# Kernel optimization log

Measured on AMD Instinct MI355X. Metric: run time of the kernel, lower is better.

## Reference

```python
import jax, jax.numpy as jnp
import numpy as np

K = 3          # k_size
STRIDE = 2
LAMDA = 10.0
PAD = K // 2
EPS = 1e-6


def _unfold(x, k, s, pad):
    # x: [B,C,H,W] -> [B, C*k*k, L]; matches torch.nn.functional.unfold ordering
    x = jnp.pad(x, ((0, 0), (0, 0), (pad, pad), (pad, pad)))
    B, C, Hp, Wp = x.shape
    Ho = (Hp - k) // s + 1
    Wo = (Wp - k) // s + 1
    # stack k*k shifted strided views -> [B, C, k*k, Ho, Wo], kk index = i*k + j
    cols = jnp.stack([x[:, :, i:i + s * (Ho - 1) + 1:s, j:j + s * (Wo - 1) + 1:s]
                      for i in range(k) for j in range(k)], axis=2)
    return cols.reshape(B, C * k * k, Ho * Wo)


def setup_inputs() -> dict:
    key = jax.random.key(0)
    k0, k1, k2, k3 = jax.random.split(key, 4)
    B, C, H, W = 4, 64, 64, 64
    bg_in = jax.random.normal(k0, (B, C, H, W), dtype=jnp.float32)
    fg_in = jax.random.normal(k1, (B, C, H, W), dtype=jnp.float32)
    mask = (jax.random.uniform(k2, (B, 1, H, W)) > 0.5).astype(jnp.float32)
    fuse_w = jax.random.normal(k3, (C, 2 * C, 1, 1), dtype=jnp.float32) * 0.02
    fuse_b = jnp.zeros((C,), dtype=jnp.float32)
    return {"bg_in": bg_in, "fg_in": fg_in, "mask": mask,
            "fuse_w": fuse_w, "fuse_b": fuse_b}


def reference(bg_in, fg_in, mask, fuse_w, fuse_b):
    B, C, H, W = bg_in.shape
    # mask is already [B,1,H,W] -> nearest resize is identity; expand over channels
    mask_r = jnp.broadcast_to(mask, (B, C, H, W))
    bg = bg_in * mask_r

    ub = _unfold(bg, K, STRIDE, 0)              # [B, d, L], d = C*K*K (bg patches = keys)
    L = ub.shape[-1]
    uf = _unfold(fg_in, K, 1, PAD)              # [B, d, H*W] (fg patches = queries)
    ww = uf.transpose(0, 2, 1).reshape(B, H, W, C * K * K)  # [B,H,W,d]

    k1d = jnp.sum(ub ** 2, axis=1)                       # [B,L]   ||key||^2
    wwd = jnp.sum(ww ** 2, axis=-1, keepdims=True)       # [B,H,W,1] ||query||^2
    CS = jnp.einsum('bhwd,bdl->bhwl', ww, ub)            # cross-correlation
    DS1 = k1d[:, None, None, :] + wwd - 2.0 * CS         # squared L2 distances [B,H,W,L]

    mean = DS1.mean(axis=-1, keepdims=True)
    std = DS1.std(axis=-1, keepdims=True)                # ddof=0 == unbiased=False
    DS2 = -jnp.tanh((DS1 - mean) / (std + EPS))
    CA = jax.nn.softmax(LAMDA * DS2, axis=-1)            # attention over L patches

    # conv_transpose2d(CA, k2, stride=1, padding=PAD): scatter-add of weighted patches
    k2 = ub.transpose(0, 2, 1).reshape(B, L, C, K, K)    # per-batch deconv weights
    T = jnp.einsum('bhwl,blcij->bchwij', CA, k2)         # [B,C,H,W,K,K]
    outp = jnp.zeros((B, C, H + 2 * PAD, W + 2 * PAD), dtype=bg_in.dtype)
    for i in range(K):
        for j in range(K):
            outp = outp.at[:, :, i:i + H, j:j + W].add(T[:, :, :, :, i, j])
    ACL = outp[:, :, PAD:PAD + H, PAD:PAD + W] / (K * K)

    ACL = bg + ACL * (1.0 - mask_r)
    con1 = jnp.concatenate([bg_in, ACL], axis=1)         # [B,2C,H,W]
    out = jnp.einsum('bdhw,cd->bchw', con1, fuse_w[:, :, 0, 0]) + fuse_b[None, :, None, None]
    return jax.nn.elu(out)
```

## Files before the change

### kernel.cpp

```cpp
#include <hip/hip_runtime.h>

#define B_   4
#define C_   64
#define HW_  4096
#define D_   576
#define L_   961
#define LP_  1024
#define LAMDA_ 10.0f
#define EPS_   1e-6f

typedef short short8 __attribute__((ext_vector_type(8)));
typedef float f32x16 __attribute__((ext_vector_type(16)));
typedef unsigned short u16;

__device__ __forceinline__ u16 f2bf(float x) {
    unsigned u = __float_as_uint(x);
    u += 0x7FFFu + ((u >> 16) & 1u);
    return (u16)(u >> 16);
}
__device__ __forceinline__ float bf2f(u16 h) {
    return __uint_as_float(((unsigned)h) << 16);
}
__device__ __forceinline__ void mfma_bf16(f32x16& d, short8 a, short8 b) {
    asm volatile("v_mfma_f32_32x32x16_bf16 %0, %1, %2, %0"
                 : "+v"(d) : "v"(a), "v"(b));
}

__global__ __launch_bounds__(256) void fill_ub_kernel(const float* __restrict__ bg_in,
                                                      const float* __restrict__ mask,
                                                      u16* __restrict__ UBh,
                                                      u16* __restrict__ UBl) {
    int idx = blockIdx.x * 256 + threadIdx.x;
    int b   = idx / (D_ * LP_);
    int rem = idx - b * (D_ * LP_);
    int d   = rem >> 10;
    int l   = idx & (LP_ - 1);
    float v = 0.f;
    if (l < L_) {
        int ly = l / 31, lx = l - ly * 31;
        int c  = d / 9,  kk = d - c * 9;
        int i  = kk / 3, j  = kk - i * 3;
        int pix = ((2 * ly + i) << 6) + 2 * lx + j;
        v = bg_in[((b * C_ + c) << 12) + pix] * mask[(b << 12) + pix];
    }
    u16 h = f2bf(v);
    UBh[idx] = h;
    UBl[idx] = f2bf(v - bf2f(h));
}

__global__ __launch_bounds__(256) void fill_ubT_kernel(const float* __restrict__ bg_in,
                                                       const float* __restrict__ mask,
                                                       u16* __restrict__ UBTh,
                                                       u16* __restrict__ UBTl) {
    int idx = blockIdx.x * 256 + threadIdx.x;
    int d   = idx % D_;
    int tmp = idx / D_;
    int l   = tmp & (LP_ - 1);
    int b   = tmp >> 10;
    float v = 0.f;
    if (l < L_) {
        int ly = l / 31, lx = l - ly * 31;
        int c  = d / 9,  kk = d - c * 9;
        int i  = kk / 3, j  = kk - i * 3;
        int pix = ((2 * ly + i) << 6) + 2 * lx + j;
        v = bg_in[((b * C_ + c) << 12) + pix] * mask[(b << 12) + pix];
    }
    u16 h = f2bf(v);
    UBTh[idx] = h;
    UBTl[idx] = f2bf(v - bf2f(h));
}

__global__ __launch_bounds__(256) void k1d_kernel(const u16* __restrict__ UBh,
                                                  const u16* __restrict__ UBl,
                                                  float* __restrict__ K1D) {
    int t = blockIdx.x * 256 + threadIdx.x;
    int b = t >> 10;
    int l = t & 1023;
    size_t base = (size_t)b * (D_ * LP_) + (size_t)(blockIdx.y * 144) * LP_ + l;
    float s = 0.f;
    #pragma unroll 8
    for (int d = 0; d < 144; ++d) {
        float v = bf2f(UBh[base + (size_t)d * LP_]) + bf2f(UBl[base + (size_t)d * LP_]);
        s += v * v;
    }
    atomicAdd(&K1D[t], s);
}

__global__ __launch_bounds__(256) void fill_ww_kernel(const float* __restrict__ fg,
                                                      u16* __restrict__ WWh,
                                                      u16* __restrict__ WWl) {
    int idx = blockIdx.x * 256 + threadIdx.x;
    int d   = idx % D_;
    int tmp = idx / D_;
    int p   = tmp & 4095;
    int b   = tmp >> 12;
    int c   = d / 9,  kk = d - c * 9;
    int i   = kk / 3, j  = kk - i * 3;
    int y   = (p >> 6) + i - 1, x = (p & 63) + j - 1;
    float v = 0.f;
    if ((unsigned)y < 64u && (unsigned)x < 64u)
        v = fg[((b * C_ + c) << 12) + (y << 6) + x];
    u16 h = f2bf(v);
    WWh[idx] = h;
    WWl[idx] = f2bf(v - bf2f(h));
}

__global__ __launch_bounds__(256) void pixsq_kernel(const float* __restrict__ fg,
                                                    float* __restrict__ P) {
    int t = blockIdx.x * 256 + threadIdx.x;
    int b = t >> 12, p = t & 4095;
    const float* base = fg + ((size_t)(b * C_) << 12) + p;
    float s = 0.f;
    #pragma unroll 8
    for (int c = 0; c < C_; ++c) { float v = base[c << 12]; s += v * v; }
    P[t] = s;
}

__global__ __launch_bounds__(256) void gemm1_kernel(
    const u16* __restrict__ WWh, const u16* __restrict__ WWl,
    const u16* __restrict__ UBTh, const u16* __restrict__ UBTl,
    float* __restrict__ CS)
{
    int b = blockIdx.z;
    const u16* Ahg = WWh  + (size_t)b * HW_ * D_;
    const u16* Alg = WWl  + (size_t)b * HW_ * D_;
    const u16* Bhg = UBTh + (size_t)b * LP_ * D_;
    const u16* Blg = UBTl + (size_t)b * LP_ * D_;
    float* C = CS + (size_t)b * HW_ * LP_;
    int n0 = blockIdx.x << 7, m0 = blockIdx.y << 7;

    __shared__ __align__(16) u16 Ah[4096], Al[4096], Bh[4096], Bl[4096];

    int t = threadIdx.x;
    int lane = t & 63;
    int w = t >> 6, wm = w >> 1, wn = w & 1;
    int lr = lane & 31, lk = lane >> 5;

    f32x16 acc[2][2];
    #pragma unroll
    for (int i = 0; i < 2; ++i)
        #pragma unroll
        for (int j = 0; j < 2; ++j)
            #pragma unroll
            for (int r = 0; r < 16; ++r) acc[i][j][r] = 0.f;

    for (int k0 = 0; k0 < D_; k0 += 32) {
        __syncthreads();
        #pragma unroll
        for (int i = 0; i < 2; ++i) {
            int lin = i * 256 + t;
            int q = lin >> 7, r = lin & 127;
            size_t ga = (size_t)(m0 + r) * D_ + k0 + q * 8;
            size_t gb = (size_t)(n0 + r) * D_ + k0 + q * 8;
            *(uint4*)&Ah[lin * 8] = *(const uint4*)(Ahg + ga);
            *(uint4*)&Al[lin * 8] = *(const uint4*)(Alg + ga);
            *(uint4*)&Bh[lin * 8] = *(const uint4*)(Bhg + gb);
            *(uint4*)&Bl[lin * 8] = *(const uint4*)(Blg + gb);
        }
        __syncthreads();
        #pragma unroll
        for (int kh = 0; kh < 2; ++kh) {
            int qq = kh * 2 + lk;
            short8 ah[2], al[2], bhf[2], blf[2];
            #pragma unroll
            for (int f = 0; f < 2; ++f) {
                int ra = (qq * 128 + wm * 64 + f * 32 + lr) * 8;
                int rb = (qq * 128 + wn * 64 + f * 32 + lr) * 8;
                ah[f]  = *(const short8*)&Ah[ra];
                al[f]  = *(const short8*)&Al[ra];
                bhf[f] = *(const short8*)&Bh[rb];
                blf[f] = *(const short8*)&Bl[rb];
            }
            #pragma unroll
            for (int fm = 0; fm < 2; ++fm)
                #pragma unroll
                for (int fn = 0; fn < 2; ++fn)
                    mfma_bf16(acc[fm][fn], ah[fm], bhf[fn]);
            #pragma unroll
            for (int fm = 0; fm < 2; ++fm)
                #pragma unroll
                for (int fn = 0; fn < 2; ++fn)
                    mfma_bf16(acc[fm][fn], ah[fm], blf[fn]);
            #pragma unroll
            for (int fm = 0; fm < 2; ++fm)
                #pragma unroll
                for (int fn = 0; fn < 2; ++fn)
                    mfma_bf16(acc[fm][fn], al[fm], bhf[fn]);
        }
    }
    #pragma unroll
    for (int fm = 0; fm < 2; ++fm)
        #pragma unroll
        for (int fn = 0; fn < 2; ++fn) {
            int colb = n0 + wn * 64 + fn * 32 + lr;
            int rowb = m0 + wm * 64 + fm * 32 + 4 * lk;
            #pragma unroll
            for (int r = 0; r < 16; ++r) {
                int row = rowb + (r & 3) + 8 * (r >> 2);
                C[(size_t)row * LP_ + colb] = acc[fm][fn][r];
            }
        }
}

__device__ __forceinline__ float block_reduce_sum(float v, float* sred) {
    #pragma unroll
    for (int m = 32; m > 0; m >>= 1) v += __shfl_xor(v, m, 64);
    __syncthreads();
    if ((threadIdx.x & 63) == 0) sred[threadIdx.x >> 6] = v;
    __syncthreads();
    return sred[0] + sred[1] + sred[2] + sred[3];
}

__global__ __launch_bounds__(256) void stats_softmax_kernel(float* __restrict__ CA,
                                                            const float* __restrict__ K1D,
                                                            const float* __restrict__ P) {
    __shared__ float sred[4];
    int row = blockIdx.x;
    int b = row >> 12, q = row & 4095;
    int h = q >> 6, wx = q & 63;
    float wwd = 0.f;
    #pragma unroll
    for (int i = 0; i < 3; ++i)
        #pragma unroll
        for (int j = 0; j < 3; ++j) {
            int y = h + i - 1, x = wx + j - 1;
            if ((unsigned)y < 64u && (unsigned)x < 64u)
                wwd += P[(b << 12) + (y << 6) + x];
        }
    float* cs = CA + (size_t)row * LP_;
    u16* ch = (u16*)cs;
    const float* k1 = K1D + (b << 10);
    int t = threadIdx.x;
    float xv[4];
    float lsum = 0.f;
    #pragma unroll
    for (int i = 0; i < 4; ++i) {
        int l = t + (i << 8);
        float ds = 0.f;
        if (l < L_) ds = k1[l] + wwd - 2.f * cs[l];
        xv[i] = ds;
        lsum += ds;
    }
    float mean = block_reduce_sum(lsum, sred) * (1.f / 961.f);
    float lvar = 0.f;
    #pragma unroll
    for (int i = 0; i < 4; ++i) {
        int l = t + (i << 8);
        if (l < L_) { float dd = xv[i] - mean; lvar += dd * dd; }
    }
    float var = block_reduce_sum(lvar, sred) * (1.f / 961.f);
    float inv = 1.f / (sqrtf(var) + EPS_);
    float ev[4];
    float lsume = 0.f;
    #pragma unroll
    for (int i = 0; i < 4; ++i) {
        int l = t + (i << 8);
        float e = 0.f;
        if (l < L_) e = expf(-LAMDA_ * tanhf((xv[i] - mean) * inv));
        ev[i] = e;
        lsume += e;
    }
    float rs = 1.f / block_reduce_sum(lsume, sred);
    #pragma unroll
    for (int i = 0; i < 4; ++i) {
        int l2 = t + (i << 8);
        float v = ev[i] * rs;
        u16 hi = f2bf(v);
        ch[l2]        = hi;
        ch[1024 + l2] = f2bf(v - bf2f(hi));
    }
}

__global__ __launch_bounds__(256) void gemm2_kernel(
    const u16* __restrict__ UBh, const u16* __restrict__ UBl,
    const float* __restrict__ CAbase, float* __restrict__ ET)
{
    int b = blockIdx.z;
    const u16* Ahg = UBh + (size_t)b * D_ * LP_;
    const u16* Alg = UBl + (size_t)b * D_ * LP_;
    const u16* CAB = (const u16*)(CAbase + (size_t)b * HW_ * LP_);
    float* C = ET + (size_t)b * D_ * HW_;
    int n0 = blockIdx.x << 8, m0 = blockIdx.y << 6;

    __shared__ __align__(16) u16 Ah[2048], Al[2048], Bh[8192], Bl[8192];

    int t = threadIdx.x;
    int lane = t & 63;
    int w = t >> 6;
    int lr = lane & 31, lk = lane >> 5;

    f32x16 acc[2][2];
    #pragma unroll
    for (int i = 0; i < 2; ++i)
        #pragma unroll
        for (int j = 0; j < 2; ++j)
            #pragma unroll
            for (int r = 0; r < 16; ++r) acc[i][j][r] = 0.f;

    for (int k0 = 0; k0 < LP_; k0 += 32) {
        __syncthreads();
        {
            int q = t >> 6, r = t & 63;
            size_t ga = (size_t)(m0 + r) * LP_ + k0 + q * 8;
            *(uint4*)&Ah[t * 8] = *(const uint4*)(Ahg + ga);
            *(uint4*)&Al[t * 8] = *(const uint4*)(Alg + ga);
        }
        #pragma unroll
        for (int i = 0; i < 4; ++i) {
            int lin = i * 256 + t;
            int q = lin >> 8, r = lin & 255;
            size_t gb = (size_t)(n0 + r) * 2048 + k0 + q * 8;
            *(uint4*)&Bh[lin * 8] = *(const uint4*)(CAB + gb);
            *(uint4*)&Bl[lin * 8] = *(const uint4*)(CAB + gb + 1024);
        }
        __syncthreads();
        #pragma unroll
        for (int kh = 0; kh < 2; ++kh) {
            int qq = kh * 2 + lk;
            short8 ah[2], al[2], bhf[2], blf[2];
            #pragma unroll
            for (int f = 0; f < 2; ++f) {
                int ra = (qq * 64 + f * 32 + lr) * 8;
                int rb = (qq * 256 + w * 64 + f * 32 + lr) * 8;
                ah[f]  = *(const short8*)&Ah[ra];
                al[f]  = *(const short8*)&Al[ra];
                bhf[f] = *(const short8*)&Bh[rb];
                blf[f] = *(const short8*)&Bl[rb];
            }
            #pragma unroll
            for (int fm = 0; fm < 2; ++fm)
                #pragma unroll
                for (int fn = 0; fn < 2; ++fn)
                    mfma_bf16(acc[fm][fn], ah[fm], bhf[fn]);
            #pragma unroll
            for (int fm = 0; fm < 2; ++fm)
                #pragma unroll
                for (int fn = 0; fn < 2; ++fn)
                    mfma_bf16(acc[fm][fn], ah[fm], blf[fn]);
            #pragma unroll
            for (int fm = 0; fm < 2; ++fm)
                #pragma unroll
                for (int fn = 0; fn < 2; ++fn)
                    mfma_bf16(acc[fm][fn], al[fm], bhf[fn]);
        }
    }
    #pragma unroll
    for (int fm = 0; fm < 2; ++fm)
        #pragma unroll
        for (int fn = 0; fn < 2; ++fn) {
            int colb = n0 + w * 64 + fn * 32 + lr;
            int rowb = m0 + fm * 32 + 4 * lk;
            #pragma unroll
            for (int r = 0; r < 16; ++r) {
                int row = rowb + (r & 3) + 8 * (r >> 2);
                C[(size_t)row * HW_ + colb] = acc[fm][fn][r];
            }
        }
}

__global__ __launch_bounds__(64) void final_kernel(const float* __restrict__ ET,
                                                   const float* __restrict__ bg_in,
                                                   const float* __restrict__ mask,
                                                   const float* __restrict__ fw,
                                                   const float* __restrict__ fb,
                                                   float* __restrict__ out) {
    __shared__ float fwT[128 * 64];
    #pragma unroll 8
    for (int lin = threadIdx.x; lin < 8192; lin += 64) {
        int c = lin >> 7, c2 = lin & 127;
        fwT[(c2 << 6) + c] = fw[lin];
    }
    __syncthreads();

    int t = blockIdx.x * 64 + threadIdx.x;
    int b = t >> 12, p = t & 4095;
    int y = p >> 6, x = p & 63;
    const float* bgp = bg_in + ((size_t)(b * C_) << 12) + p;
    const float* Eb  = ET + (size_t)b * D_ * HW_;
    float m = mask[t];

    float acc[64];
    #pragma unroll
    for (int c = 0; c < 64; ++c) acc[c] = fb[c];

    for (int c2 = 0; c2 < 64; ++c2) {
        float bgv = bgp[(size_t)c2 << 12];
        float a = 0.f;
        if (m == 0.f) {
            #pragma unroll
            for (int kk = 0; kk < 9; ++kk) {
                int i = kk / 3, j = kk - (kk / 3) * 3;
                int hh = y + 1 - i, ww2 = x + 1 - j;
                if ((unsigned)hh < 64u && (unsigned)ww2 < 64u)
                    a += Eb[(size_t)(c2 * 9 + kk) * HW_ + (hh << 6) + ww2];
            }
            a *= (1.f / 9.f);
        }
        float aclv = (m != 0.f) ? bgv : a;
        const float* f1 = &fwT[c2 << 6];
        const float* f2 = &fwT[(64 + c2) << 6];
        #pragma unroll
        for (int c4 = 0; c4 < 16; ++c4) {
            float4 fa  = *(const float4*)&f1[c4 << 2];
            float4 fb4 = *(const float4*)&f2[c4 << 2];
            acc[(c4 << 2) + 0] += fa.x * bgv + fb4.x * aclv;
            acc[(c4 << 2) + 1] += fa.y * bgv + fb4.y * aclv;
            acc[(c4 << 2) + 2] += fa.z * bgv + fb4.z * aclv;
            acc[(c4 << 2) + 3] += fa.w * bgv + fb4.w * aclv;
        }
    }
    float* op = out + ((size_t)(b * C_) << 12) + p;
    #pragma unroll
    for (int c = 0; c < 64; ++c) {
        float v = acc[c];
        op[(size_t)c << 12] = v > 0.f ? v : expm1f(v);
    }
}

extern "C" void kernel_launch(void* const* d_in, const int* in_sizes, int n_in,
                              void* d_out, int out_size, void* d_ws, size_t ws_size,
                              hipStream_t stream) {
    const float* bg_in  = (const float*)d_in[0];
    const float* fg_in  = (const float*)d_in[1];
    const float* mask   = (const float*)d_in[2];
    const float* fuse_w = (const float*)d_in[3];
    const float* fuse_b = (const float*)d_in[4];
    float* out = (float*)d_out;

    char* base = (char*)d_ws;
    u16* WWh  = (u16*)base;  base += (size_t)B_ * HW_ * D_ * 2;
    u16* WWl  = (u16*)base;  base += (size_t)B_ * HW_ * D_ * 2;
    u16* UBh  = (u16*)base;  base += (size_t)B_ * D_ * LP_ * 2;
    u16* UBl  = (u16*)base;  base += (size_t)B_ * D_ * LP_ * 2;
    u16* UBTh = (u16*)base;  base += (size_t)B_ * LP_ * D_ * 2;
    u16* UBTl = (u16*)base;  base += (size_t)B_ * LP_ * D_ * 2;
    float* CS  = (float*)base;  base += (size_t)B_ * HW_ * LP_ * 4;
    float* K1D = (float*)base;  base += (size_t)B_ * LP_ * 4;
    float* P   = (float*)base;  base += (size_t)B_ * HW_ * 4;
    float* ET  = (float*)WWh;

    hipMemsetAsync(K1D, 0, (size_t)B_ * LP_ * sizeof(float), stream);
    fill_ub_kernel <<<(B_ * D_ * LP_) / 256, 256, 0, stream>>>(bg_in, mask, UBh, UBl);
    fill_ubT_kernel<<<(B_ * LP_ * D_) / 256, 256, 0, stream>>>(bg_in, mask, UBTh, UBTl);
    k1d_kernel<<<dim3((B_ * LP_) / 256, 4), 256, 0, stream>>>(UBh, UBl, K1D);
    fill_ww_kernel<<<(B_ * HW_ * D_) / 256, 256, 0, stream>>>(fg_in, WWh, WWl);
    pixsq_kernel<<<(B_ * HW_) / 256, 256, 0, stream>>>(fg_in, P);
    gemm1_kernel<<<dim3(LP_ / 128, HW_ / 128, B_), 256, 0, stream>>>(WWh, WWl, UBTh, UBTl, CS);
    stats_softmax_kernel<<<B_ * HW_, 256, 0, stream>>>(CS, K1D, P);
    gemm2_kernel<<<dim3(HW_ / 256, D_ / 64, B_), 256, 0, stream>>>(UBh, UBl, CS, ET);
    final_kernel<<<(B_ * HW_) / 64, 64, 0, stream>>>(ET, bg_in, mask, fuse_w, fuse_b, out);
}
```

Before: 667.6 us.

## Double-buffer GEMM LDS tiles with direct global-to-LDS loads; split final-kernel channels

Both MFMA GEMM kernels now use two LDS buffers and prefetch the next K-slice while computing the current one. The prefetch goes through the global_load_lds builtin when the compiler provides it, so each K step needs one barrier instead of two, and global latency overlaps with MFMA work. The final fuse/ELU kernel moves from 64-thread to 256-thread blocks, and each wave handles 16 of the 64 output channels. That adds parallelism and lowers register pressure, but every wave re-gathers the deconvolution sum for its pixel, which repeats global reads. The doubled LDS footprint (80 KB in gemm2) may also lower occupancy.

```diff
diff --git a/kernel.cpp b/kernel.cpp
--- a/kernel.cpp
+++ b/kernel.cpp
@@ -24,6 +24,16 @@
 __device__ __forceinline__ void mfma_bf16(f32x16& d, short8 a, short8 b) {
     asm volatile("v_mfma_f32_32x32x16_bf16 %0, %1, %2, %0"
                  : "+v"(d) : "v"(a), "v"(b));
+}
+
+__device__ __forceinline__ void gl16(const u16* g, u16* l) {
+#if defined(__has_builtin) && __has_builtin(__builtin_amdgcn_global_load_lds)
+    __builtin_amdgcn_global_load_lds(
+        (const __attribute__((address_space(1))) unsigned int*)g,
+        (__attribute__((address_space(3))) unsigned int*)l, 16, 0, 0);
+#else
+    *(uint4*)l = *(const uint4*)g;
+#endif
 }
 
 __global__ __launch_bounds__(256) void fill_ub_kernel(const float* __restrict__ bg_in,
@@ -116,6 +126,23 @@
     P[t] = s;
 }
 
+__device__ __forceinline__ void g1_stage(const u16* Ahg, const u16* Alg,
+                                         const u16* Bhg, const u16* Blg,
+                                         u16* sAh, u16* sAl, u16* sBh, u16* sBl,
+                                         int t, int m0, int n0, int k0) {
+    #pragma unroll
+    for (int i = 0; i < 2; ++i) {
+        int lin = i * 256 + t;
+        int q = lin >> 7, r = lin & 127;
+        size_t ga = (size_t)(m0 + r) * D_ + k0 + q * 8;
+        size_t gb = (size_t)(n0 + r) * D_ + k0 + q * 8;
+        gl16(Ahg + ga, sAh + lin * 8);
+        gl16(Alg + ga, sAl + lin * 8);
+        gl16(Bhg + gb, sBh + lin * 8);
+        gl16(Blg + gb, sBl + lin * 8);
+    }
+}
+
 __global__ __launch_bounds__(256) void gemm1_kernel(
     const u16* __restrict__ WWh, const u16* __restrict__ WWl,
     const u16* __restrict__ UBTh, const u16* __restrict__ UBTl,
@@ -129,7 +156,7 @@
     float* C = CS + (size_t)b * HW_ * LP_;
     int n0 = blockIdx.x << 7, m0 = blockIdx.y << 7;
 
-    __shared__ __align__(16) u16 Ah[4096], Al[4096], Bh[4096], Bl[4096];
+    __shared__ __align__(16) u16 Ah[2][4096], Al[2][4096], Bh[2][4096], Bl[2][4096];
 
     int t = threadIdx.x;
     int lane = t & 63;
@@ -144,20 +171,16 @@
             #pragma unroll
             for (int r = 0; r < 16; ++r) acc[i][j][r] = 0.f;
 
-    for (int k0 = 0; k0 < D_; k0 += 32) {
-        __syncthreads();
-        #pragma unroll
-        for (int i = 0; i < 2; ++i) {
-            int lin = i * 256 + t;
-            int q = lin >> 7, r = lin & 127;
-            size_t ga = (size_t)(m0 + r) * D_ + k0 + q * 8;
-            size_t gb = (size_t)(n0 + r) * D_ + k0 + q * 8;
-            *(uint4*)&Ah[lin * 8] = *(const uint4*)(Ahg + ga);
-            *(uint4*)&Al[lin * 8] = *(const uint4*)(Alg + ga);
-            *(uint4*)&Bh[lin * 8] = *(const uint4*)(Bhg + gb);
-            *(uint4*)&Bl[lin * 8] = *(const uint4*)(Blg + gb);
-        }
-        __syncthreads();
+    g1_stage(Ahg, Alg, Bhg, Blg, Ah[0], Al[0], Bh[0], Bl[0], t, m0, n0, 0);
+    __syncthreads();
+    int cur = 0;
+    for (int it = 0; it < 18; ++it) {
+        if (it < 17)
+            g1_stage(Ahg, Alg, Bhg, Blg,
+                     Ah[cur ^ 1], Al[cur ^ 1], Bh[cur ^ 1], Bl[cur ^ 1],
+                     t, m0, n0, (it + 1) * 32);
+        const u16* sAh = Ah[cur]; const u16* sAl = Al[cur];
+        const u16* sBh = Bh[cur]; const u16* sBl = Bl[cur];
         #pragma unroll
         for (int kh = 0; kh < 2; ++kh) {
             int qq = kh * 2 + lk;
@@ -166,10 +189,10 @@
             for (int f = 0; f < 2; ++f) {
                 int ra = (qq * 128 + wm * 64 + f * 32 + lr) * 8;
                 int rb = (qq * 128 + wn * 64 + f * 32 + lr) * 8;
-                ah[f]  = *(const short8*)&Ah[ra];
-                al[f]  = *(const short8*)&Al[ra];
-                bhf[f] = *(const short8*)&Bh[rb];
-                blf[f] = *(const short8*)&Bl[rb];
+                ah[f]  = *(const short8*)&sAh[ra];
+                al[f]  = *(const short8*)&sAl[ra];
+                bhf[f] = *(const short8*)&sBh[rb];
+                blf[f] = *(const short8*)&sBl[rb];
             }
             #pragma unroll
             for (int fm = 0; fm < 2; ++fm)
@@ -187,6 +210,8 @@
                 for (int fn = 0; fn < 2; ++fn)
                     mfma_bf16(acc[fm][fn], al[fm], bhf[fn]);
         }
+        __syncthreads();
+        cur ^= 1;
     }
     #pragma unroll
     for (int fm = 0; fm < 2; ++fm)
@@ -268,6 +293,26 @@
         u16 hi = f2bf(v);
         ch[l2]        = hi;
         ch[1024 + l2] = f2bf(v - bf2f(hi));
+    }
+}
+
+__device__ __forceinline__ void g2_stage(const u16* Ahg, const u16* Alg,
+                                         const u16* CAB,
+                                         u16* sAh, u16* sAl, u16* sBh, u16* sBl,
+                                         int t, int m0, int n0, int k0) {
+    {
+        int q = t >> 6, r = t & 63;
+        size_t ga = (size_t)(m0 + r) * LP_ + k0 + q * 8;
+        gl16(Ahg + ga, sAh + t * 8);
+        gl16(Alg + ga, sAl + t * 8);
+    }
+    #pragma unroll
+    for (int i = 0; i < 4; ++i) {
+        int lin = i * 256 + t;
+        int q = lin >> 8, r = lin & 255;
+        size_t gb = (size_t)(n0 + r) * 2048 + k0 + q * 8;
+        gl16(CAB + gb,        sBh + lin * 8);
+        gl16(CAB + gb + 1024, sBl + lin * 8);
     }
 }
 
@@ -282,7 +327,7 @@
     float* C = ET + (size_t)b * D_ * HW_;
     int n0 = blockIdx.x << 8, m0 = blockIdx.y << 6;
 
-    __shared__ __align__(16) u16 Ah[2048], Al[2048], Bh[8192], Bl[8192];
+    __shared__ __align__(16) u16 Ah[2][2048], Al[2][2048], Bh[2][8192], Bl[2][8192];
 
     int t = threadIdx.x;
     int lane = t & 63;
@@ -297,23 +342,16 @@
             #pragma unroll
             for (int r = 0; r < 16; ++r) acc[i][j][r] = 0.f;
 
-    for (int k0 = 0; k0 < LP_; k0 += 32) {
-        __syncthreads();
-        {
-            int q = t >> 6, r = t & 63;
-            size_t ga = (size_t)(m0 + r) * LP_ + k0 + q * 8;
-            *(uint4*)&Ah[t * 8] = *(const uint4*)(Ahg + ga);
-            *(uint4*)&Al[t * 8] = *(const uint4*)(Alg + ga);
-        }
-        #pragma unroll
-        for (int i = 0; i < 4; ++i) {
-            int lin = i * 256 + t;
-            int q = lin >> 8, r = lin & 255;
-            size_t gb = (size_t)(n0 + r) * 2048 + k0 + q * 8;
-            *(uint4*)&Bh[lin * 8] = *(const uint4*)(CAB + gb);
-            *(uint4*)&Bl[lin * 8] = *(const uint4*)(CAB + gb + 1024);
-        }
-        __syncthreads();
+    g2_stage(Ahg, Alg, CAB, Ah[0], Al[0], Bh[0], Bl[0], t, m0, n0, 0);
+    __syncthreads();
+    int cur = 0;
+    for (int it = 0; it < 32; ++it) {
+        if (it < 31)
+            g2_stage(Ahg, Alg, CAB,
+                     Ah[cur ^ 1], Al[cur ^ 1], Bh[cur ^ 1], Bl[cur ^ 1],
+                     t, m0, n0, (it + 1) * 32);
+        const u16* sAh = Ah[cur]; const u16* sAl = Al[cur];
+        const u16* sBh = Bh[cur]; const u16* sBl = Bl[cur];
         #pragma unroll
         for (int kh = 0; kh < 2; ++kh) {
             int qq = kh * 2 + lk;
@@ -322,10 +360,10 @@
             for (int f = 0; f < 2; ++f) {
                 int ra = (qq * 64 + f * 32 + lr) * 8;
                 int rb = (qq * 256 + w * 64 + f * 32 + lr) * 8;
-                ah[f]  = *(const short8*)&Ah[ra];
-                al[f]  = *(const short8*)&Al[ra];
-                bhf[f] = *(const short8*)&Bh[rb];
-                blf[f] = *(const short8*)&Bl[rb];
+                ah[f]  = *(const short8*)&sAh[ra];
+                al[f]  = *(const short8*)&sAl[ra];
+                bhf[f] = *(const short8*)&sBh[rb];
+                blf[f] = *(const short8*)&sBl[rb];
             }
             #pragma unroll
             for (int fm = 0; fm < 2; ++fm)
@@ -343,6 +381,8 @@
                 for (int fn = 0; fn < 2; ++fn)
                     mfma_bf16(acc[fm][fn], al[fm], bhf[fn]);
         }
+        __syncthreads();
+        cur ^= 1;
     }
     #pragma unroll
     for (int fm = 0; fm < 2; ++fm)
@@ -358,30 +398,34 @@
         }
 }
 
-__global__ __launch_bounds__(64) void final_kernel(const float* __restrict__ ET,
-                                                   const float* __restrict__ bg_in,
-                                                   const float* __restrict__ mask,
-                                                   const float* __restrict__ fw,
-                                                   const float* __restrict__ fb,
-                                                   float* __restrict__ out) {
+__global__ __launch_bounds__(256) void final_kernel(const float* __restrict__ ET,
+                                                    const float* __restrict__ bg_in,
+                                                    const float* __restrict__ mask,
+                                                    const float* __restrict__ fw,
+                                                    const float* __restrict__ fb,
+                                                    float* __restrict__ out) {
     __shared__ float fwT[128 * 64];
-    #pragma unroll 8
-    for (int lin = threadIdx.x; lin < 8192; lin += 64) {
+    #pragma unroll
+    for (int i = 0; i < 32; ++i) {
+        int lin = i * 256 + threadIdx.x;
         int c = lin >> 7, c2 = lin & 127;
         fwT[(c2 << 6) + c] = fw[lin];
     }
     __syncthreads();
 
-    int t = blockIdx.x * 64 + threadIdx.x;
-    int b = t >> 12, p = t & 4095;
+    int qc = threadIdx.x >> 6;
+    int px = threadIdx.x & 63;
+    int gp = blockIdx.x * 64 + px;
+    int b = gp >> 12, p = gp & 4095;
     int y = p >> 6, x = p & 63;
     const float* bgp = bg_in + ((size_t)(b * C_) << 12) + p;
     const float* Eb  = ET + (size_t)b * D_ * HW_;
-    float m = mask[t];
-
-    float acc[64];
-    #pragma unroll
-    for (int c = 0; c < 64; ++c) acc[c] = fb[c];
+    float m = mask[gp];
+    int c0 = qc << 4;
+
+    float acc[16];
+    #pragma unroll
+    for (int c = 0; c < 16; ++c) acc[c] = fb[c0 + c];
 
     for (int c2 = 0; c2 < 64; ++c2) {
         float bgv = bgp[(size_t)c2 << 12];
@@ -397,10 +441,10 @@
             a *= (1.f / 9.f);
         }
         float aclv = (m != 0.f) ? bgv : a;
-        const float* f1 = &fwT[c2 << 6];
-        const float* f2 = &fwT[(64 + c2) << 6];
-        #pragma unroll
-        for (int c4 = 0; c4 < 16; ++c4) {
+        const float* f1 = &fwT[(c2 << 6) + c0];
+        const float* f2 = &fwT[((64 + c2) << 6) + c0];
+        #pragma unroll
+        for (int c4 = 0; c4 < 4; ++c4) {
             float4 fa  = *(const float4*)&f1[c4 << 2];
             float4 fb4 = *(const float4*)&f2[c4 << 2];
             acc[(c4 << 2) + 0] += fa.x * bgv + fb4.x * aclv;
@@ -411,9 +455,9 @@
     }
     float* op = out + ((size_t)(b * C_) << 12) + p;
     #pragma unroll
-    for (int c = 0; c < 64; ++c) {
+    for (int c = 0; c < 16; ++c) {
         float v = acc[c];
-        op[(size_t)c << 12] = v > 0.f ? v : expm1f(v);
+        op[(size_t)(c0 + c) << 12] = v > 0.f ? v : expm1f(v);
     }
 }
 
@@ -448,5 +492,5 @@
     gemm1_kernel<<<dim3(LP_ / 128, HW_ / 128, B_), 256, 0, stream>>>(WWh, WWl, UBTh, UBTl, CS);
     stats_softmax_kernel<<<B_ * HW_, 256, 0, stream>>>(CS, K1D, P);
     gemm2_kernel<<<dim3(HW_ / 256, D_ / 64, B_), 256, 0, stream>>>(UBh, UBl, CS, ET);
-    final_kernel<<<(B_ * HW_) / 64, 64, 0, stream>>>(ET, bg_in, mask, fuse_w, fuse_b, out);
-}
+    final_kernel<<<(B_ * HW_) / 64, 256, 0, stream>>>(ET, bg_in, mask, fuse_w, fuse_b, out);
+}
```

Result: faster. 633.2 us (-5.2%).

## Load GEMM tiles directly into LDS, shrink gemm2 tile, split final-kernel channels

Applied to the files above, without the earlier changes.

Both MFMA GEMM kernels now stage their tiles with global_load_lds (direct global-to-LDS copies) instead of loading into registers and then storing to shared memory. The barrier is moved to the end of each k-iteration. gemm2 uses a 64x128 block tile with one N fragment per wave, which doubles the grid. final_kernel now runs 256 threads per block, with four groups each computing 16 of the 64 output channels, to raise occupancy and cut registers per thread. The costs are that the neighbourhood gathers of ET and bg are repeated four times per pixel, and that correctness depends on the direct-to-LDS builtin's wave-uniform addressing and on the compiler waiting for outstanding loads before the barrier.

```diff
diff --git a/kernel.cpp b/kernel.cpp
--- a/kernel.cpp
+++ b/kernel.cpp
@@ -24,6 +24,16 @@
 __device__ __forceinline__ void mfma_bf16(f32x16& d, short8 a, short8 b) {
     asm volatile("v_mfma_f32_32x32x16_bf16 %0, %1, %2, %0"
                  : "+v"(d) : "v"(a), "v"(b));
+}
+
+__device__ __forceinline__ void gl16(const u16* g, u16* l) {
+#if defined(__has_builtin) && __has_builtin(__builtin_amdgcn_global_load_lds)
+    __builtin_amdgcn_global_load_lds(
+        (const __attribute__((address_space(1))) unsigned int*)g,
+        (__attribute__((address_space(3))) unsigned int*)l, 16, 0, 0);
+#else
+    *(uint4*)l = *(const uint4*)g;
+#endif
 }
 
 __global__ __launch_bounds__(256) void fill_ub_kernel(const float* __restrict__ bg_in,
@@ -145,17 +155,16 @@
             for (int r = 0; r < 16; ++r) acc[i][j][r] = 0.f;
 
     for (int k0 = 0; k0 < D_; k0 += 32) {
-        __syncthreads();
         #pragma unroll
         for (int i = 0; i < 2; ++i) {
             int lin = i * 256 + t;
             int q = lin >> 7, r = lin & 127;
             size_t ga = (size_t)(m0 + r) * D_ + k0 + q * 8;
             size_t gb = (size_t)(n0 + r) * D_ + k0 + q * 8;
-            *(uint4*)&Ah[lin * 8] = *(const uint4*)(Ahg + ga);
-            *(uint4*)&Al[lin * 8] = *(const uint4*)(Alg + ga);
-            *(uint4*)&Bh[lin * 8] = *(const uint4*)(Bhg + gb);
-            *(uint4*)&Bl[lin * 8] = *(const uint4*)(Blg + gb);
+            gl16(Ahg + ga, Ah + lin * 8);
+            gl16(Alg + ga, Al + lin * 8);
+            gl16(Bhg + gb, Bh + lin * 8);
+            gl16(Blg + gb, Bl + lin * 8);
         }
         __syncthreads();
         #pragma unroll
@@ -187,6 +196,7 @@
                 for (int fn = 0; fn < 2; ++fn)
                     mfma_bf16(acc[fm][fn], al[fm], bhf[fn]);
         }
+        __syncthreads();
     }
     #pragma unroll
     for (int fm = 0; fm < 2; ++fm)
@@ -280,108 +290,101 @@
     const u16* Alg = UBl + (size_t)b * D_ * LP_;
     const u16* CAB = (const u16*)(CAbase + (size_t)b * HW_ * LP_);
     float* C = ET + (size_t)b * D_ * HW_;
-    int n0 = blockIdx.x << 8, m0 = blockIdx.y << 6;
-
-    __shared__ __align__(16) u16 Ah[2048], Al[2048], Bh[8192], Bl[8192];
+    int n0 = blockIdx.x << 7, m0 = blockIdx.y << 6;
+
+    __shared__ __align__(16) u16 Ah[2048], Al[2048], Bh[4096], Bl[4096];
 
     int t = threadIdx.x;
     int lane = t & 63;
     int w = t >> 6;
     int lr = lane & 31, lk = lane >> 5;
 
-    f32x16 acc[2][2];
+    f32x16 acc[2];
     #pragma unroll
     for (int i = 0; i < 2; ++i)
         #pragma unroll
-        for (int j = 0; j < 2; ++j)
-            #pragma unroll
-            for (int r = 0; r < 16; ++r) acc[i][j][r] = 0.f;
+        for (int r = 0; r < 16; ++r) acc[i][r] = 0.f;
 
     for (int k0 = 0; k0 < LP_; k0 += 32) {
-        __syncthreads();
         {
             int q = t >> 6, r = t & 63;
             size_t ga = (size_t)(m0 + r) * LP_ + k0 + q * 8;
-            *(uint4*)&Ah[t * 8] = *(const uint4*)(Ahg + ga);
-            *(uint4*)&Al[t * 8] = *(const uint4*)(Alg + ga);
-        }
-        #pragma unroll
-        for (int i = 0; i < 4; ++i) {
+            gl16(Ahg + ga, Ah + t * 8);
+            gl16(Alg + ga, Al + t * 8);
+        }
+        #pragma unroll
+        for (int i = 0; i < 2; ++i) {
             int lin = i * 256 + t;
-            int q = lin >> 8, r = lin & 255;
+            int q = lin >> 7, r = lin & 127;
             size_t gb = (size_t)(n0 + r) * 2048 + k0 + q * 8;
-            *(uint4*)&Bh[lin * 8] = *(const uint4*)(CAB + gb);
-            *(uint4*)&Bl[lin * 8] = *(const uint4*)(CAB + gb + 1024);
+            gl16(CAB + gb,        Bh + lin * 8);
+            gl16(CAB + gb + 1024, Bl + lin * 8);
         }
         __syncthreads();
         #pragma unroll
         for (int kh = 0; kh < 2; ++kh) {
             int qq = kh * 2 + lk;
-            short8 ah[2], al[2], bhf[2], blf[2];
+            short8 ah[2], al[2], bhf, blf;
             #pragma unroll
             for (int f = 0; f < 2; ++f) {
                 int ra = (qq * 64 + f * 32 + lr) * 8;
-                int rb = (qq * 256 + w * 64 + f * 32 + lr) * 8;
-                ah[f]  = *(const short8*)&Ah[ra];
-                al[f]  = *(const short8*)&Al[ra];
-                bhf[f] = *(const short8*)&Bh[rb];
-                blf[f] = *(const short8*)&Bl[rb];
+                ah[f] = *(const short8*)&Ah[ra];
+                al[f] = *(const short8*)&Al[ra];
             }
-            #pragma unroll
-            for (int fm = 0; fm < 2; ++fm)
-                #pragma unroll
-                for (int fn = 0; fn < 2; ++fn)
-                    mfma_bf16(acc[fm][fn], ah[fm], bhf[fn]);
-            #pragma unroll
-            for (int fm = 0; fm < 2; ++fm)
-                #pragma unroll
-                for (int fn = 0; fn < 2; ++fn)
-                    mfma_bf16(acc[fm][fn], ah[fm], blf[fn]);
-            #pragma unroll
-            for (int fm = 0; fm < 2; ++fm)
-                #pragma unroll
-                for (int fn = 0; fn < 2; ++fn)
-                    mfma_bf16(acc[fm][fn], al[fm], bhf[fn]);
-        }
-    }
-    #pragma unroll
-    for (int fm = 0; fm < 2; ++fm)
-        #pragma unroll
-        for (int fn = 0; fn < 2; ++fn) {
-            int colb = n0 + w * 64 + fn * 32 + lr;
-            int rowb = m0 + fm * 32 + 4 * lk;
-            #pragma unroll
-            for (int r = 0; r < 16; ++r) {
-                int row = rowb + (r & 3) + 8 * (r >> 2);
-                C[(size_t)row * HW_ + colb] = acc[fm][fn][r];
+            {
+                int rb = (qq * 128 + w * 32 + lr) * 8;
+                bhf = *(const short8*)&Bh[rb];
+                blf = *(const short8*)&Bl[rb];
             }
-        }
-}
-
-__global__ __launch_bounds__(64) void final_kernel(const float* __restrict__ ET,
-                                                   const float* __restrict__ bg_in,
-                                                   const float* __restrict__ mask,
-                                                   const float* __restrict__ fw,
-                                                   const float* __restrict__ fb,
-                                                   float* __restrict__ out) {
+            #pragma unroll
+            for (int fm = 0; fm < 2; ++fm) mfma_bf16(acc[fm], ah[fm], bhf);
+            #pragma unroll
+            for (int fm = 0; fm < 2; ++fm) mfma_bf16(acc[fm], ah[fm], blf);
+            #pragma unroll
+            for (int fm = 0; fm < 2; ++fm) mfma_bf16(acc[fm], al[fm], bhf);
+        }
+        __syncthreads();
+    }
+    #pragma unroll
+    for (int fm = 0; fm < 2; ++fm) {
+        int colb = n0 + w * 32 + lr;
+        int rowb = m0 + fm * 32 + 4 * lk;
+        #pragma unroll
+        for (int r = 0; r < 16; ++r) {
+            int row = rowb + (r & 3) + 8 * (r >> 2);
+            C[(size_t)row * HW_ + colb] = acc[fm][r];
+        }
+    }
+}
+
+__global__ __launch_bounds__(256) void final_kernel(const float* __restrict__ ET,
+                                                    const float* __restrict__ bg_in,
+                                                    const float* __restrict__ mask,
+                                                    const float* __restrict__ fw,
+                                                    const float* __restrict__ fb,
+                                                    float* __restrict__ out) {
     __shared__ float fwT[128 * 64];
-    #pragma unroll 8
-    for (int lin = threadIdx.x; lin < 8192; lin += 64) {
+    #pragma unroll
+    for (int i = 0; i < 32; ++i) {
+        int lin = i * 256 + threadIdx.x;
         int c = lin >> 7, c2 = lin & 127;
         fwT[(c2 << 6) + c] = fw[lin];
     }
     __syncthreads();
 
-    int t = blockIdx.x * 64 + threadIdx.x;
-    int b = t >> 12, p = t & 4095;
+    int qc = threadIdx.x >> 6;
+    int px = threadIdx.x & 63;
+    int gp = blockIdx.x * 64 + px;
+    int b = gp >> 12, p = gp & 4095;
     int y = p >> 6, x = p & 63;
     const float* bgp = bg_in + ((size_t)(b * C_) << 12) + p;
     const float* Eb  = ET + (size_t)b * D_ * HW_;
-    float m = mask[t];
-
-    float acc[64];
-    #pragma unroll
-    for (int c = 0; c < 64; ++c) acc[c] = fb[c];
+    float m = mask[gp];
+    int c0 = qc << 4;
+
+    float acc[16];
+    #pragma unroll
+    for (int c = 0; c < 16; ++c) acc[c] = fb[c0 + c];
 
     for (int c2 = 0; c2 < 64; ++c2) {
         float bgv = bgp[(size_t)c2 << 12];
@@ -397,10 +400,10 @@
             a *= (1.f / 9.f);
         }
         float aclv = (m != 0.f) ? bgv : a;
-        const float* f1 = &fwT[c2 << 6];
-        const float* f2 = &fwT[(64 + c2) << 6];
-        #pragma unroll
-        for (int c4 = 0; c4 < 16; ++c4) {
+        const float* f1 = &fwT[(c2 << 6) + c0];
+        const float* f2 = &fwT[((64 + c2) << 6) + c0];
+        #pragma unroll
+        for (int c4 = 0; c4 < 4; ++c4) {
             float4 fa  = *(const float4*)&f1[c4 << 2];
             float4 fb4 = *(const float4*)&f2[c4 << 2];
             acc[(c4 << 2) + 0] += fa.x * bgv + fb4.x * aclv;
@@ -411,9 +414,9 @@
     }
     float* op = out + ((size_t)(b * C_) << 12) + p;
     #pragma unroll
-    for (int c = 0; c < 64; ++c) {
+    for (int c = 0; c < 16; ++c) {
         float v = acc[c];
-        op[(size_t)c << 12] = v > 0.f ? v : expm1f(v);
+        op[(size_t)(c0 + c) << 12] = v > 0.f ? v : expm1f(v);
     }
 }
 
@@ -447,6 +450,6 @@
     pixsq_kernel<<<(B_ * HW_) / 256, 256, 0, stream>>>(fg_in, P);
     gemm1_kernel<<<dim3(LP_ / 128, HW_ / 128, B_), 256, 0, stream>>>(WWh, WWl, UBTh, UBTl, CS);
     stats_softmax_kernel<<<B_ * HW_, 256, 0, stream>>>(CS, K1D, P);
-    gemm2_kernel<<<dim3(HW_ / 256, D_ / 64, B_), 256, 0, stream>>>(UBh, UBl, CS, ET);
-    final_kernel<<<(B_ * HW_) / 64, 64, 0, stream>>>(ET, bg_in, mask, fuse_w, fuse_b, out);
-}
+    gemm2_kernel<<<dim3(HW_ / 128, D_ / 64, B_), 256, 0, stream>>>(UBh, UBl, CS, ET);
+    final_kernel<<<(B_ * HW_) / 64, 256, 0, stream>>>(ET, bg_in, mask, fuse_w, fuse_b, out);
+}
```

Result: faster. 561.2 us (-15.9%).
